# Performance work log

Measured on AMD Instinct MI355X. Metric: run time of the kernel, lower is better.

The kernel has to match this reference:

```python
import jax, jax.numpy as jnp
import numpy as np

N_HEAD = 8
D_HEAD = 32  # d_model=256 // n_head=8
SCALE = 1.0 / (D_HEAD ** 0.5)
CLIP = 10.0


def _rel_shift(x):
    # x: [qlen, klen, B, nh]; Transformer-XL relative shift along axis 1
    qlen, klen = x.shape[0], x.shape[1]
    zero_pad = jnp.zeros((qlen, 1) + x.shape[2:], dtype=x.dtype)
    x_pad = jnp.concatenate([zero_pad, x], axis=1)          # [qlen, klen+1, B, nh]
    x_pad = x_pad.reshape((klen + 1, qlen) + x.shape[2:])   # row-major reshape (torch .view)
    return x_pad[1:].reshape(x.shape)


def setup_inputs() -> dict:
    key = jax.random.key(0)
    ks = jax.random.split(key, 7)
    S, B, H = 1024, 8, 256
    return {
        "q": jax.random.normal(ks[0], (S, B, H), dtype=jnp.float32),
        "k": jax.random.normal(ks[1], (S, B, H), dtype=jnp.float32),
        "v": jax.random.normal(ks[2], (S, B, H), dtype=jnp.float32),
        "r": jax.random.normal(ks[3], (S, 1, H), dtype=jnp.float32),
        "bias_u": jax.random.normal(ks[4], (N_HEAD, D_HEAD), dtype=jnp.float32),
        "bias_v": jax.random.normal(ks[5], (N_HEAD, D_HEAD), dtype=jnp.float32),
        "mask": jax.random.randint(ks[6], (S, S, B), 0, 2).astype(jnp.bool_),
    }


def reference(q, k, v, r, bias_u, bias_v, mask):
    qlen, bsz = q.shape[0], q.shape[1]
    klen, rlen = k.shape[0], r.shape[0]
    q = q.reshape(qlen, bsz, N_HEAD, D_HEAD)
    k = k.reshape(klen, bsz, N_HEAD, D_HEAD)
    v = v.reshape(klen, bsz, N_HEAD, D_HEAD)
    r = r.reshape(rlen, N_HEAD, D_HEAD)

    AC = jnp.einsum('ibnd,jbnd->ijbn', q + bias_u, k)   # content term
    BD = jnp.einsum('ibnd,jnd->ijbn', q + bias_v, r)    # position term
    BD = _rel_shift(BD)

    score = (AC + BD) * SCALE
    score = CLIP * jnp.tanh(score)                      # clip > 0 path

    weight = jax.nn.softmax(score, axis=1)              # softmax over klen

    # mask is not None path: masked softmax of head-mean logits
    logits = score.mean(axis=-1)                        # [qlen, klen, B]
    logits = jnp.where(mask, -jnp.inf, logits)
    probs = jax.nn.softmax(logits, axis=1)

    out = jnp.einsum('ijbn,jbnd->ibnd', weight, v)
    out = out.reshape(qlen, bsz, N_HEAD * D_HEAD)
    return out, probs
```

## Files before the change

### kernel.cpp

```cpp
#include <hip/hip_runtime.h>
#include <hip/hip_fp16.h>

#define S 1024
#define B 8
#define NH 8
#define DH 32
#define HID 256
#define SCALEF 0.17677669529663687f

typedef __attribute__((ext_vector_type(8))) _Float16 f16x8;
typedef __attribute__((ext_vector_type(4))) _Float16 f16x4;
typedef __attribute__((ext_vector_type(4))) float f32x4;
#define MFMAH(a, b, c) __builtin_amdgcn_mfma_f32_16x16x32_f16(a, b, c, 0, 0, 0)

#define OFF_K_H 0
#define OFF_K_L 2560
#define OFF_VT  5120
#define OFF_RL  7680
#define OFF_RH  12800
#define OFF_P   17920
#define LDS_HF  20480

#define C_E2  0.51006978f
#define C_PWA 14.42695041f
#define C_PWB -28.85390082f

__device__ __forceinline__ void splitf16_4(const float4 x, _Float16* dh, _Float16* dl) {
  f16x4 h, l;
  h.x = (_Float16)x.x; h.y = (_Float16)x.y; h.z = (_Float16)x.z; h.w = (_Float16)x.w;
  l.x = (_Float16)(x.x - (float)h.x); l.y = (_Float16)(x.y - (float)h.y);
  l.z = (_Float16)(x.z - (float)h.z); l.w = (_Float16)(x.w - (float)h.w);
  *(f16x4*)dh = h; *(f16x4*)dl = l;
}
__device__ __forceinline__ void cvtf16_4(const float4 x, _Float16* d) {
  f16x4 h;
  h.x = (_Float16)x.x; h.y = (_Float16)x.y; h.z = (_Float16)x.z; h.w = (_Float16)x.w;
  *(f16x4*)d = h;
}

__global__ __launch_bounds__(256)
void relattn_mfma_86028194939537(const float* __restrict__ q, const float* __restrict__ k,
                                 const float* __restrict__ v, const float* __restrict__ r,
                                 const float* __restrict__ bu, const float* __restrict__ bv,
                                 float* __restrict__ out, __half* __restrict__ sws) {
  __shared__ _Float16 sm[LDS_HF];
  const int t = threadIdx.x;
  const int lane = t & 63, w = t >> 6;
  const int quad = lane >> 4, jn = lane & 15;
  const int bid = blockIdx.x;
  const int b = bid & 7, it = (bid >> 3) & 15, n = bid >> 7;
  const int i0 = it << 6, iw0 = i0 + (w << 4);
  const int colq = quad << 3;
  const int i16 = i0 >> 4;

  f16x8 qu_h, qu_l, qv_h, qv_l, qn_h, qn_l;
  {
    const float* bup = bu + n * DH + colq;
    const float* bvp = bv + n * DH + colq;
    const float* qp = q + (size_t)(iw0 + jn) * 2048 + b * HID + n * DH + colq;
    int r1 = iw0 + 1 + jn; if (r1 > S - 1) r1 = S - 1;
    const float* qp1 = q + (size_t)r1 * 2048 + b * HID + n * DH + colq;
#pragma unroll
    for (int e = 0; e < 8; ++e) {
      float xu = qp[e] + bup[e], xv = qp[e] + bvp[e], xn = qp1[e] + bvp[e];
      _Float16 h;
      h = (_Float16)xu; qu_h[e] = h; qu_l[e] = (_Float16)(xu - (float)h);
      h = (_Float16)xv; qv_h[e] = h; qv_l[e] = (_Float16)(xv - (float)h);
      h = (_Float16)xn; qn_h[e] = h; qn_l[e] = (_Float16)(xn - (float)h);
    }
  }

  const int prow = lane >> 2, pseg = lane & 3;
  __half* swsp = sws + (((size_t)(iw0 + prow) * 8 + b) * 8 + n) * 1024 + (pseg << 3);

  f32x4 out0 = {0.f, 0.f, 0.f, 0.f}, out1 = {0.f, 0.f, 0.f, 0.f};
  float ls[4] = {0.f, 0.f, 0.f, 0.f};

  {
    int j = t >> 3, d4 = (t & 7) << 2;
    const size_t g = (size_t)j * 2048 + b * HID + n * DH + d4;
    float4 kx = *(const float4*)(k + g);
    float4 vx = *(const float4*)(v + g);
    splitf16_4(kx, &sm[OFF_K_H + j * 40 + d4], &sm[OFF_K_L + j * 40 + d4]);
    sm[OFF_VT + (d4 + 0) * 40 + j] = (_Float16)vx.x;
    sm[OFF_VT + (d4 + 1) * 40 + j] = (_Float16)vx.y;
    sm[OFF_VT + (d4 + 2) * 40 + j] = (_Float16)vx.z;
    sm[OFF_VT + (d4 + 3) * 40 + j] = (_Float16)vx.w;
  }
#pragma unroll
  for (int p = 0; p < 3; ++p) {
    int ti = 2 * p + (t >> 7), row = (t >> 3) & 15, d4 = (t & 7) << 2;
    {
      int kL = 60 - i16 + ti;
      int tg = (kL << 4) + row; tg = tg < 0 ? 0 : (tg > S - 1 ? S - 1 : tg);
      float4 rv = *(const float4*)(r + (size_t)tg * HID + n * DH + d4);
      int sl = (kL + 72) & 7;
      cvtf16_4(rv, &sm[OFF_RL + (sl * 16 + row) * 40 + d4]);
    }
    {
      int kH = -i16 - 3 + ti;
      int tg = (kH << 4) - 17 + row; tg = tg < 0 ? 0 : (tg > S - 1 ? S - 1 : tg);
      float4 rv = *(const float4*)(r + (size_t)tg * HID + n * DH + d4);
      int sl = (kH + 72) & 7;
      cvtf16_4(rv, &sm[OFF_RH + (sl * 16 + row) * 40 + d4]);
    }
  }

  for (int jt = 0; jt < 32; ++jt) {
    const int j0 = jt << 5;
    __syncthreads();

    if (jt < 31) {
      int j = t >> 3, d4 = (t & 7) << 2;
      const int nbuf = ((jt + 1) & 1) * 1280;
      const size_t g = (size_t)(j0 + 32 + j) * 2048 + b * HID + n * DH + d4;
      float4 kx = *(const float4*)(k + g);
      float4 vx = *(const float4*)(v + g);
      splitf16_4(kx, &sm[OFF_K_H + nbuf + j * 40 + d4], &sm[OFF_K_L + nbuf + j * 40 + d4]);
      sm[OFF_VT + nbuf + (d4 + 0) * 40 + j] = (_Float16)vx.x;
      sm[OFF_VT + nbuf + (d4 + 1) * 40 + j] = (_Float16)vx.y;
      sm[OFF_VT + nbuf + (d4 + 2) * 40 + j] = (_Float16)vx.z;
      sm[OFF_VT + nbuf + (d4 + 3) * 40 + j] = (_Float16)vx.w;
    }
    {
      int ti = t >> 7, row = (t >> 3) & 15, d4 = (t & 7) << 2;
      {
        int kL = 66 + 2 * jt - i16 + ti;
        int tg = (kL << 4) + row; tg = tg < 0 ? 0 : (tg > S - 1 ? S - 1 : tg);
        float4 rv = *(const float4*)(r + (size_t)tg * HID + n * DH + d4);
        int sl = (kL + 72) & 7;
        cvtf16_4(rv, &sm[OFF_RL + (sl * 16 + row) * 40 + d4]);
      }
      {
        int kH = 2 * jt - i16 + 3 + ti;
        int tg = (kH << 4) - 17 + row; tg = tg < 0 ? 0 : (tg > S - 1 ? S - 1 : tg);
        float4 rv = *(const float4*)(r + (size_t)tg * HID + n * DH + d4);
        int sl = (kH + 72) & 7;
        cvtf16_4(rv, &sm[OFF_RH + (sl * 16 + row) * 40 + d4]);
      }
    }

    const int buf = (jt & 1) * 1280;
    const bool lowA = (j0 <= iw0 + 15);
    const bool highA = (j0 + 29 >= iw0);

    f32x4 ac0 = {0.f, 0.f, 0.f, 0.f}, ac1 = {0.f, 0.f, 0.f, 0.f};
    {
      f16x8 b0h = *(const f16x8*)&sm[OFF_K_H + buf + jn * 40 + colq];
      f16x8 b0l = *(const f16x8*)&sm[OFF_K_L + buf + jn * 40 + colq];
      f16x8 b1h = *(const f16x8*)&sm[OFF_K_H + buf + (16 + jn) * 40 + colq];
      f16x8 b1l = *(const f16x8*)&sm[OFF_K_L + buf + (16 + jn) * 40 + colq];
      ac0 = MFMAH(qu_h, b0h, ac0); ac0 = MFMAH(qu_h, b0l, ac0); ac0 = MFMAH(qu_l, b0h, ac0);
      ac1 = MFMAH(qu_h, b1h, ac1); ac1 = MFMAH(qu_h, b1l, ac1); ac1 = MFMAH(qu_l, b1h, ac1);
    }

    f32x4 zl0 = {0.f,0.f,0.f,0.f}, zl1 = {0.f,0.f,0.f,0.f}, zl2 = {0.f,0.f,0.f,0.f};
    f32x4 zh0 = {0.f,0.f,0.f,0.f}, zh1 = {0.f,0.f,0.f,0.f}, zh2 = {0.f,0.f,0.f,0.f};
    if (lowA) {
#pragma unroll
      for (int z = 0; z < 3; ++z) {
        int kL = 63 - i16 - w + 2 * jt + z;
        int sl = (kL + 72) & 7;
        f16x8 rr = *(const f16x8*)&sm[OFF_RL + (sl * 16 + jn) * 40 + colq];
        f32x4 acc = {0.f, 0.f, 0.f, 0.f};
        acc = MFMAH(qv_h, rr, acc); acc = MFMAH(qv_l, rr, acc);
        if (z == 0) zl0 = acc; else if (z == 1) zl1 = acc; else zl2 = acc;
      }
    }
    if (highA) {
#pragma unroll
      for (int z = 0; z < 3; ++z) {
        int kH = 2 * jt - i16 - w + z;
        int sl = (kH + 72) & 7;
        f16x8 rr = *(const f16x8*)&sm[OFF_RH + (sl * 16 + jn) * 40 + colq];
        f32x4 acc = {0.f, 0.f, 0.f, 0.f};
        acc = MFMAH(qn_h, rr, acc); acc = MFMAH(qn_l, rr, acc);
        if (z == 0) zh0 = acc; else if (z == 1) zh1 = acc; else zh2 = acc;
      }
    }

#pragma unroll
    for (int g = 0; g < 4; ++g) {
      const int qr = (quad << 2) + g;
      const int c0 = 15 - qr + jn;
      const int src = (lane & 48) | (c0 & 15);
      const bool zs = (c0 < 16);
      float lo0 = 0.f, lo1 = 0.f, hv0 = 0.f, hv1 = 0.f;
      if (lowA) {
        float a0 = __shfl(zl0[g], src, 64);
        float a1 = __shfl(zl1[g], src, 64);
        float a2 = __shfl(zl2[g], src, 64);
        lo0 = zs ? a0 : a1; lo1 = zs ? a1 : a2;
      }
      if (highA) {
        float a0 = __shfl(zh0[g], src, 64);
        float a1 = __shfl(zh1[g], src, 64);
        float a2 = __shfl(zh2[g], src, 64);
        hv0 = zs ? a0 : a1; hv1 = zs ? a1 : a2;
      }
      const int dj0 = j0 + jn - iw0 - qr;
#pragma unroll
      for (int f = 0; f < 2; ++f) {
        const int dj = dj0 + (f << 4);
        const float bd = (dj <= 0) ? (f ? lo1 : lo0) : ((dj == 1) ? 0.f : (f ? hv1 : hv0));
        const float acv = f ? ac1[g] : ac0[g];
        const float s = acv + bd;
        const float e2 = __builtin_amdgcn_exp2f(s * C_E2);
        const float tq = __builtin_amdgcn_rcpf(e2 + 1.f);
        const float pw = __builtin_amdgcn_exp2f(fmaf(tq, C_PWB, C_PWA));
        const _Float16 ph = (_Float16)pw;
        ls[g] += (float)ph;
        sm[OFF_P + w * 640 + qr * 40 + (f << 4) + jn] = ph;
      }
    }

    {
      f16x8 pa = *(const f16x8*)&sm[OFF_P + w * 640 + jn * 40 + colq];
      f16x8 v0 = *(const f16x8*)&sm[OFF_VT + buf + jn * 40 + colq];
      f16x8 v1 = *(const f16x8*)&sm[OFF_VT + buf + (16 + jn) * 40 + colq];
      out0 = MFMAH(pa, v0, out0);
      out1 = MFMAH(pa, v1, out1);
    }

    {
      f16x8 pr = *(const f16x8*)&sm[OFF_P + w * 640 + prow * 40 + (pseg << 3)];
      *(f16x8*)swsp = pr;
      swsp += 32;
    }
  }

#pragma unroll
  for (int g = 0; g < 4; ++g) {
    float s = ls[g];
    s += __shfl_xor(s, 1, 64); s += __shfl_xor(s, 2, 64);
    s += __shfl_xor(s, 4, 64); s += __shfl_xor(s, 8, 64);
    const float inv = 1.0f / s;
    const int qr = (quad << 2) + g;
    float* op = out + (size_t)(iw0 + qr) * 2048 + b * HID + n * DH;
    op[jn] = out0[g] * inv;
    op[16 + jn] = out1[g] * inv;
  }
}

__global__ __launch_bounds__(1024)
void relattn_probs_86028194939537(const __half* __restrict__ sws, const int* __restrict__ mask,
                                  float* __restrict__ probs) {
  __shared__ _Float16 ebuf[8][1032];
  __shared__ unsigned char mb[8192];
  __shared__ float psum[8][4];
  __shared__ float binv[8];
  const int t = threadIdx.x;
  const int i = blockIdx.x;
  const int tj = t & 255, bg = t >> 8;
  const int j4 = tj << 2;
  const int wl = (t >> 6) & 3;

  {
    const int4* m4 = (const int4*)(mask + (size_t)i * 8192);
#pragma unroll
    for (int u = 0; u < 2; ++u) {
      int idx = t + (u << 10);
      int4 mv = m4[idx];
      uchar4 mbv;
      mbv.x = (unsigned char)(mv.x != 0); mbv.y = (unsigned char)(mv.y != 0);
      mbv.z = (unsigned char)(mv.z != 0); mbv.w = (unsigned char)(mv.w != 0);
      *(uchar4*)&mb[idx << 2] = mbv;
    }
  }
  __syncthreads();

#pragma unroll
  for (int bb = 0; bb < 2; ++bb) {
    const int b = (bg << 1) + bb;
    float a0 = 1.f, a1 = 1.f, a2 = 1.f, a3 = 1.f;
#pragma unroll
    for (int n = 0; n < 8; ++n) {
      f16x4 pv = *(const f16x4*)(sws + (((size_t)i * 8 + b) * 8 + n) * 1024 + j4);
      a0 *= (float)pv.x; a1 *= (float)pv.y; a2 *= (float)pv.z; a3 *= (float)pv.w;
    }
    float e0 = mb[(j4 + 0) * 8 + b] ? 0.f : sqrtf(sqrtf(sqrtf(a0)));
    float e1 = mb[(j4 + 1) * 8 + b] ? 0.f : sqrtf(sqrtf(sqrtf(a1)));
    float e2 = mb[(j4 + 2) * 8 + b] ? 0.f : sqrtf(sqrtf(sqrtf(a2)));
    float e3 = mb[(j4 + 3) * 8 + b] ? 0.f : sqrtf(sqrtf(sqrtf(a3)));
    f16x4 ev;
    ev.x = (_Float16)e0; ev.y = (_Float16)e1; ev.z = (_Float16)e2; ev.w = (_Float16)e3;
    *(f16x4*)&ebuf[b][j4] = ev;
    float s = ((float)ev.x + (float)ev.y) + ((float)ev.z + (float)ev.w);
#pragma unroll
    for (int off = 32; off > 0; off >>= 1) s += __shfl_xor(s, off, 64);
    if ((t & 63) == 0) psum[b][wl] = s;
  }
  __syncthreads();
  if (t < 8) binv[t] = 1.0f / (psum[t][0] + psum[t][1] + psum[t][2] + psum[t][3]);
  __syncthreads();
#pragma unroll
  for (int u = 0; u < 2; ++u) {
    int f0 = (t << 2) + (u << 12);
    float4 o;
    o.x = (float)ebuf[(f0 + 0) & 7][(f0 + 0) >> 3] * binv[(f0 + 0) & 7];
    o.y = (float)ebuf[(f0 + 1) & 7][(f0 + 1) >> 3] * binv[(f0 + 1) & 7];
    o.z = (float)ebuf[(f0 + 2) & 7][(f0 + 2) >> 3] * binv[(f0 + 2) & 7];
    o.w = (float)ebuf[(f0 + 3) & 7][(f0 + 3) >> 3] * binv[(f0 + 3) & 7];
    *(float4*)(probs + (size_t)i * 8192 + f0) = o;
  }
}

#define TI 8
#define TJ 8
#define NTILE (S / TJ)
#define KSTR 288
#define KOFF 0
#define VOFF (TJ * KSTR)
#define BAND (2 * TJ * KSTR)
#define PROWS (TI + TJ - 1)
#define BSTR 292
#define BVR (BAND + PROWS * BSTR)
#define BUKo (BVR + PROWS * 8)
#define LDS_FL (BUKo + 64)

__global__ __launch_bounds__(256, 2)
void relattn_main_fb(const float* __restrict__ q, const float* __restrict__ k,
                     const float* __restrict__ v, const float* __restrict__ r,
                     const float* __restrict__ bias_u, const float* __restrict__ bias_v,
                     const int* __restrict__ mask, float* __restrict__ out,
                     float* __restrict__ probs_raw, float* __restrict__ ws_logits, int use_ws) {
  __shared__ float smf[LDS_FL];
  const int t = threadIdx.x;
  const int n = t & 7;
  const int il = (t >> 3) & 7;
  const int jp = t >> 6;
  const int bid = blockIdx.x;
  const int b = bid & 7;
  const int i0 = (bid >> 3) * TI;
  const int i = i0 + il;
  float qq[DH], qn[DH];
  {
    const float4* qr = (const float4*)(q + (i * B + b) * HID + n * DH);
#pragma unroll
    for (int dd = 0; dd < 8; ++dd) {
      float4 a = qr[dd];
      qq[4*dd+0] = a.x; qq[4*dd+1] = a.y; qq[4*dd+2] = a.z; qq[4*dd+3] = a.w;
    }
    if (i + 1 < S) {
      const float4* q2 = (const float4*)(q + ((i + 1) * B + b) * HID + n * DH);
#pragma unroll
      for (int dd = 0; dd < 8; ++dd) {
        float4 a = q2[dd];
        qn[4*dd+0] = a.x; qn[4*dd+1] = a.y; qn[4*dd+2] = a.z; qn[4*dd+3] = a.w;
      }
    } else {
#pragma unroll
      for (int d = 0; d < DH; ++d) qn[d] = 0.f;
    }
  }
  float oacc[DH];
#pragma unroll
  for (int d = 0; d < DH; ++d) oacc[d] = 0.f;
  float lsum = 0.f;
  for (int jt = 0; jt < NTILE; ++jt) {
    const int j0 = jt * TJ;
    const int Pstar = i0 + (TI - 1) - j0;
    const int lowBase = S - TI + j0 - i0;
    const int upBase = j0 - i0 - (TI + 1);
    __syncthreads();
    {
      int u = t;
      int row = u >> 6, c = u & 63;
      int gofs = ((j0 + row) * B + b) * HID + c * 4;
      int lofs = row * KSTR + (c >> 3) * 36 + (c & 7) * 4;
      *(float4*)(smf + KOFF + lofs) = *(const float4*)(k + gofs);
      *(float4*)(smf + VOFF + lofs) = *(const float4*)(v + gofs);
      u = t + 256; row = u >> 6; c = u & 63;
      gofs = ((j0 + row) * B + b) * HID + c * 4;
      lofs = row * KSTR + (c >> 3) * 36 + (c & 7) * 4;
      *(float4*)(smf + KOFF + lofs) = *(const float4*)(k + gofs);
      *(float4*)(smf + VOFF + lofs) = *(const float4*)(v + gofs);
    }
    for (int u = t; u < PROWS * 64; u += 256) {
      int prow = u >> 6, c = u & 63;
      int trow = (prow <= Pstar) ? (lowBase + prow) : (upBase + prow);
      float4 val = make_float4(0.f, 0.f, 0.f, 0.f);
      if ((unsigned)trow < (unsigned)S) val = *(const float4*)(r + trow * HID + c * 4);
      *(float4*)(smf + BAND + prow * BSTR + (c >> 3) * 36 + (c & 7) * 4) = val;
    }
    if (t < 64 + PROWS * 8) {
      const float4 *bb, *src;
      int slot;
      bool zero = false;
      if (t < 64) {
        int jl = t >> 3, nn = t & 7;
        bb = (const float4*)(bias_u + nn * DH);
        src = (const float4*)(k + ((j0 + jl) * B + b) * HID + nn * DH);
        slot = BUKo + jl * 8 + nn;
      } else {
        int u2 = t - 64;
        int prow = u2 >> 3, nn = u2 & 7;
        int trow = (prow <= Pstar) ? (lowBase + prow) : (upBase + prow);
        bb = (const float4*)(bias_v + nn * DH);
        if ((unsigned)trow < (unsigned)S) src = (const float4*)(r + trow * HID + nn * DH);
        else { src = bb; zero = true; }
        slot = BVR + prow * 8 + nn;
      }
      float a0 = 0.f, a1 = 0.f, a2 = 0.f, a3 = 0.f;
#pragma unroll
      for (int dd = 0; dd < 8; ++dd) {
        float4 x = bb[dd], y = src[dd];
        a0 = fmaf(x.x, y.x, a0); a1 = fmaf(x.y, y.y, a1);
        a2 = fmaf(x.z, y.z, a2); a3 = fmaf(x.w, y.w, a3);
      }
      smf[slot] = zero ? 0.f : ((a0 + a1) + (a2 + a3));
    }
    __syncthreads();
#pragma unroll
    for (int jj = 0; jj < 2; ++jj) {
      const int jl = jp * 2 + jj;
      const int jg = j0 + jl;
      const int p = jl + (TI - 1) - il;
      float a0 = 0.f, a1 = 0.f, a2 = 0.f, a3 = 0.f;
      const float4* kr = (const float4*)(smf + KOFF + jl * KSTR + n * 36);
#pragma unroll
      for (int dd = 0; dd < 8; ++dd) {
        float4 kv = kr[dd];
        a0 = fmaf(qq[4*dd+0], kv.x, a0); a1 = fmaf(qq[4*dd+1], kv.y, a1);
        a2 = fmaf(qq[4*dd+2], kv.z, a2); a3 = fmaf(qq[4*dd+3], kv.w, a3);
      }
      float ac = (a0 + a1) + (a2 + a3) + smf[BUKo + jl * 8 + n];
      float b0 = 0.f, b1 = 0.f, b2 = 0.f, b3 = 0.f;
      const float4* br = (const float4*)(smf + BAND + p * BSTR + n * 36);
      if (jg <= i) {
#pragma unroll
        for (int dd = 0; dd < 8; ++dd) {
          float4 bv4 = br[dd];
          b0 = fmaf(qq[4*dd+0], bv4.x, b0); b1 = fmaf(qq[4*dd+1], bv4.y, b1);
          b2 = fmaf(qq[4*dd+2], bv4.z, b2); b3 = fmaf(qq[4*dd+3], bv4.w, b3);
        }
      } else {
#pragma unroll
        for (int dd = 0; dd < 8; ++dd) {
          float4 bv4 = br[dd];
          b0 = fmaf(qn[4*dd+0], bv4.x, b0); b1 = fmaf(qn[4*dd+1], bv4.y, b1);
          b2 = fmaf(qn[4*dd+2], bv4.z, b2); b3 = fmaf(qn[4*dd+3], bv4.w, b3);
        }
      }
      float bd = (b0 + b1) + (b2 + b3) + smf[BVR + p * 8 + n];
      float sr = (ac + bd) * SCALEF;
      sr = fminf(fmaxf(sr, -15.f), 15.f);
      float e2 = __expf(2.f * sr);
      float scv = 10.f * (e2 - 1.f) / (e2 + 1.f);
      float ssum = scv;
      ssum += __shfl_xor(ssum, 1, 64);
      ssum += __shfl_xor(ssum, 2, 64);
      ssum += __shfl_xor(ssum, 4, 64);
      if (n == 0) {
        float logit = ssum * 0.125f;
        if (use_ws) {
          ws_logits[(i * B + b) * S + jg] = logit;
        } else {
          int gofs = (i * S + jg) * B + b;
          probs_raw[gofs] = (mask[gofs] != 0) ? -1e30f : logit;
        }
      }
      float pw = __expf(scv);
      lsum += pw;
      const float4* vr = (const float4*)(smf + VOFF + jl * KSTR + n * 36);
#pragma unroll
      for (int dd = 0; dd < 8; ++dd) {
        float4 vv = vr[dd];
        oacc[4*dd+0] = fmaf(pw, vv.x, oacc[4*dd+0]);
        oacc[4*dd+1] = fmaf(pw, vv.y, oacc[4*dd+1]);
        oacc[4*dd+2] = fmaf(pw, vv.z, oacc[4*dd+2]);
        oacc[4*dd+3] = fmaf(pw, vv.w, oacc[4*dd+3]);
      }
    }
  }
  __syncthreads();
  if (jp >= 2) {
    float* red = smf + (t - 128) * 33;
#pragma unroll
    for (int d = 0; d < DH; ++d) red[d] = oacc[d];
    red[DH] = lsum;
  }
  __syncthreads();
  if (jp < 2) {
    const float* red = smf + t * 33;
#pragma unroll
    for (int d = 0; d < DH; ++d) oacc[d] += red[d];
    lsum += red[DH];
  }
  __syncthreads();
  if (jp == 1) {
    float* red = smf + (t - 64) * 33;
#pragma unroll
    for (int d = 0; d < DH; ++d) red[d] = oacc[d];
    red[DH] = lsum;
  }
  __syncthreads();
  if (jp == 0) {
    const float* red = smf + t * 33;
#pragma unroll
    for (int d = 0; d < DH; ++d) oacc[d] += red[d];
    lsum += red[DH];
    float inv = 1.f / lsum;
    float4* orow = (float4*)(out + (i * B + b) * HID + n * DH);
#pragma unroll
    for (int dd = 0; dd < 8; ++dd) {
      float4 o4;
      o4.x = oacc[4*dd+0] * inv; o4.y = oacc[4*dd+1] * inv;
      o4.z = oacc[4*dd+2] * inv; o4.w = oacc[4*dd+3] * inv;
      orow[dd] = o4;
    }
  }
}

__global__ __launch_bounds__(256)
void relattn_norm_fb(float* __restrict__ probs, const float* __restrict__ ws_logits,
                     const int* __restrict__ mask, int use_ws) {
  const int t = threadIdx.x;
  const int bid = blockIdx.x;
  const int b = bid & 7;
  const int i = bid >> 3;
  float vals[4];
  float s = 0.f;
#pragma unroll
  for (int kk = 0; kk < 4; ++kk) {
    int j = t + 256 * kk;
    float lg;
    if (use_ws) {
      lg = ws_logits[(i * B + b) * S + j];
      if (mask[(i * S + j) * B + b] != 0) lg = -1e30f;
    } else {
      lg = probs[(i * S + j) * B + b];
    }
    vals[kk] = __expf(lg);
    s += vals[kk];
  }
#pragma unroll
  for (int off = 32; off > 0; off >>= 1) s += __shfl_down(s, off, 64);
  __shared__ float wsum[4];
  __shared__ float tot;
  if ((t & 63) == 0) wsum[t >> 6] = s;
  __syncthreads();
  if (t == 0) tot = wsum[0] + wsum[1] + wsum[2] + wsum[3];
  __syncthreads();
  float inv = 1.f / tot;
#pragma unroll
  for (int kk = 0; kk < 4; ++kk) {
    int j = t + 256 * kk;
    probs[(i * S + j) * B + b] = vals[kk] * inv;
  }
}

extern "C" void kernel_launch(void* const* d_in, const int* in_sizes, int n_in,
                              void* d_out, int out_size, void* d_ws, size_t ws_size,
                              hipStream_t stream) {
  const float* q  = (const float*)d_in[0];
  const float* k  = (const float*)d_in[1];
  const float* v  = (const float*)d_in[2];
  const float* r  = (const float*)d_in[3];
  const float* bu = (const float*)d_in[4];
  const float* bv = (const float*)d_in[5];
  const int* mask = (const int*)d_in[6];
  float* out = (float*)d_out;
  float* probs = out + S * B * HID;

  const size_t WS_NEED = (size_t)S * S * B * NH * sizeof(__half);
  if (ws_size >= WS_NEED) {
    __half* sws = (__half*)d_ws;
    relattn_mfma_86028194939537<<<dim3(1024), dim3(256), 0, stream>>>(
        q, k, v, r, bu, bv, out, sws);
    relattn_probs_86028194939537<<<dim3(1024), dim3(1024), 0, stream>>>(sws, mask, probs);
  } else {
    float* wsl = (float*)d_ws;
    const int use_ws = (ws_size >= (size_t)S * S * B * sizeof(float)) ? 1 : 0;
    relattn_main_fb<<<dim3((S / TI) * B), dim3(256), 0, stream>>>(
        q, k, v, r, bu, bv, mask, out, probs, wsl, use_ws);
    relattn_norm_fb<<<dim3(S * B), dim3(256), 0, stream>>>(probs, wsl, mask, use_ws);
  }
}
```

Measured before the change: 286.0 us.

## Swizzle V transpose in LDS, skip unused R tiles, reduce shuffles, add priorities

Applies an XOR swizzle to the transposed V tile in LDS, on both the write and the read side, to reduce bank conflicts on the scattered per-element stores. It also skips loading R tiles for the low and high diagonals when later iterations will not use them. Before each cross-lane shuffle it selects between neighbouring accumulators, so each shuffle step does two shuffles instead of three. It wraps the MFMA sections in s_setprio hints. The risks are that the swizzle mapping must match exactly between writer and reader, and that the new skip conditions must cover every tile the compute loop reads.

```diff
diff --git a/kernel.cpp b/kernel.cpp
--- a/kernel.cpp
+++ b/kernel.cpp
@@ -53,6 +53,13 @@
   const int colq = quad << 3;
   const int i16 = i0 >> 4;
 
+  const int jstage = t >> 3, dstage = (t & 7) << 2;
+  const int jsw = jstage ^ ((t & 3) << 3);
+  const int vcolsw = colq ^ (((jn >> 2) & 3) << 3);
+
+  const int jtL_last = (i0 + 63) >> 5;
+  const bool proH = (i0 <= 125);
+
   f16x8 qu_h, qu_l, qv_h, qv_l, qn_h, qn_l;
   {
     const float* bup = bu + n * DH + colq;
@@ -77,15 +84,14 @@
   float ls[4] = {0.f, 0.f, 0.f, 0.f};
 
   {
-    int j = t >> 3, d4 = (t & 7) << 2;
-    const size_t g = (size_t)j * 2048 + b * HID + n * DH + d4;
+    const size_t g = (size_t)jstage * 2048 + b * HID + n * DH + dstage;
     float4 kx = *(const float4*)(k + g);
     float4 vx = *(const float4*)(v + g);
-    splitf16_4(kx, &sm[OFF_K_H + j * 40 + d4], &sm[OFF_K_L + j * 40 + d4]);
-    sm[OFF_VT + (d4 + 0) * 40 + j] = (_Float16)vx.x;
-    sm[OFF_VT + (d4 + 1) * 40 + j] = (_Float16)vx.y;
-    sm[OFF_VT + (d4 + 2) * 40 + j] = (_Float16)vx.z;
-    sm[OFF_VT + (d4 + 3) * 40 + j] = (_Float16)vx.w;
+    splitf16_4(kx, &sm[OFF_K_H + jstage * 40 + dstage], &sm[OFF_K_L + jstage * 40 + dstage]);
+    sm[OFF_VT + (dstage + 0) * 40 + jsw] = (_Float16)vx.x;
+    sm[OFF_VT + (dstage + 1) * 40 + jsw] = (_Float16)vx.y;
+    sm[OFF_VT + (dstage + 2) * 40 + jsw] = (_Float16)vx.z;
+    sm[OFF_VT + (dstage + 3) * 40 + jsw] = (_Float16)vx.w;
   }
 #pragma unroll
   for (int p = 0; p < 3; ++p) {
@@ -97,7 +103,7 @@
       int sl = (kL + 72) & 7;
       cvtf16_4(rv, &sm[OFF_RL + (sl * 16 + row) * 40 + d4]);
     }
-    {
+    if (proH) {
       int kH = -i16 - 3 + ti;
       int tg = (kH << 4) - 17 + row; tg = tg < 0 ? 0 : (tg > S - 1 ? S - 1 : tg);
       float4 rv = *(const float4*)(r + (size_t)tg * HID + n * DH + d4);
@@ -111,27 +117,27 @@
     __syncthreads();
 
     if (jt < 31) {
-      int j = t >> 3, d4 = (t & 7) << 2;
       const int nbuf = ((jt + 1) & 1) * 1280;
-      const size_t g = (size_t)(j0 + 32 + j) * 2048 + b * HID + n * DH + d4;
+      const size_t g = (size_t)(j0 + 32 + jstage) * 2048 + b * HID + n * DH + dstage;
       float4 kx = *(const float4*)(k + g);
       float4 vx = *(const float4*)(v + g);
-      splitf16_4(kx, &sm[OFF_K_H + nbuf + j * 40 + d4], &sm[OFF_K_L + nbuf + j * 40 + d4]);
-      sm[OFF_VT + nbuf + (d4 + 0) * 40 + j] = (_Float16)vx.x;
-      sm[OFF_VT + nbuf + (d4 + 1) * 40 + j] = (_Float16)vx.y;
-      sm[OFF_VT + nbuf + (d4 + 2) * 40 + j] = (_Float16)vx.z;
-      sm[OFF_VT + nbuf + (d4 + 3) * 40 + j] = (_Float16)vx.w;
+      splitf16_4(kx, &sm[OFF_K_H + nbuf + jstage * 40 + dstage],
+                 &sm[OFF_K_L + nbuf + jstage * 40 + dstage]);
+      sm[OFF_VT + nbuf + (dstage + 0) * 40 + jsw] = (_Float16)vx.x;
+      sm[OFF_VT + nbuf + (dstage + 1) * 40 + jsw] = (_Float16)vx.y;
+      sm[OFF_VT + nbuf + (dstage + 2) * 40 + jsw] = (_Float16)vx.z;
+      sm[OFF_VT + nbuf + (dstage + 3) * 40 + jsw] = (_Float16)vx.w;
     }
     {
       int ti = t >> 7, row = (t >> 3) & 15, d4 = (t & 7) << 2;
-      {
+      if (jt <= jtL_last) {
         int kL = 66 + 2 * jt - i16 + ti;
         int tg = (kL << 4) + row; tg = tg < 0 ? 0 : (tg > S - 1 ? S - 1 : tg);
         float4 rv = *(const float4*)(r + (size_t)tg * HID + n * DH + d4);
         int sl = (kL + 72) & 7;
         cvtf16_4(rv, &sm[OFF_RL + (sl * 16 + row) * 40 + d4]);
       }
-      {
+      if (32 * jt >= i0 - 125) {
         int kH = 2 * jt - i16 + 3 + ti;
         int tg = (kH << 4) - 17 + row; tg = tg < 0 ? 0 : (tg > S - 1 ? S - 1 : tg);
         float4 rv = *(const float4*)(r + (size_t)tg * HID + n * DH + d4);
@@ -144,6 +150,7 @@
     const bool lowA = (j0 <= iw0 + 15);
     const bool highA = (j0 + 29 >= iw0);
 
+    __builtin_amdgcn_s_setprio(1);
     f32x4 ac0 = {0.f, 0.f, 0.f, 0.f}, ac1 = {0.f, 0.f, 0.f, 0.f};
     {
       f16x8 b0h = *(const f16x8*)&sm[OFF_K_H + buf + jn * 40 + colq];
@@ -178,25 +185,26 @@
         if (z == 0) zh0 = acc; else if (z == 1) zh1 = acc; else zh2 = acc;
       }
     }
+    __builtin_amdgcn_s_setprio(0);
 
 #pragma unroll
     for (int g = 0; g < 4; ++g) {
       const int qr = (quad << 2) + g;
       const int c0 = 15 - qr + jn;
       const int src = (lane & 48) | (c0 & 15);
-      const bool zs = (c0 < 16);
+      const bool pred = (jn >= 15 - qr);
       float lo0 = 0.f, lo1 = 0.f, hv0 = 0.f, hv1 = 0.f;
       if (lowA) {
-        float a0 = __shfl(zl0[g], src, 64);
-        float a1 = __shfl(zl1[g], src, 64);
-        float a2 = __shfl(zl2[g], src, 64);
-        lo0 = zs ? a0 : a1; lo1 = zs ? a1 : a2;
+        float vA = pred ? zl0[g] : zl1[g];
+        float vB = pred ? zl1[g] : zl2[g];
+        lo0 = __shfl(vA, src, 64);
+        lo1 = __shfl(vB, src, 64);
       }
       if (highA) {
-        float a0 = __shfl(zh0[g], src, 64);
-        float a1 = __shfl(zh1[g], src, 64);
-        float a2 = __shfl(zh2[g], src, 64);
-        hv0 = zs ? a0 : a1; hv1 = zs ? a1 : a2;
+        float vA = pred ? zh0[g] : zh1[g];
+        float vB = pred ? zh1[g] : zh2[g];
+        hv0 = __shfl(vA, src, 64);
+        hv1 = __shfl(vB, src, 64);
       }
       const int dj0 = j0 + jn - iw0 - qr;
 #pragma unroll
@@ -214,13 +222,15 @@
       }
     }
 
+    __builtin_amdgcn_s_setprio(1);
     {
       f16x8 pa = *(const f16x8*)&sm[OFF_P + w * 640 + jn * 40 + colq];
-      f16x8 v0 = *(const f16x8*)&sm[OFF_VT + buf + jn * 40 + colq];
-      f16x8 v1 = *(const f16x8*)&sm[OFF_VT + buf + (16 + jn) * 40 + colq];
+      f16x8 v0 = *(const f16x8*)&sm[OFF_VT + buf + jn * 40 + vcolsw];
+      f16x8 v1 = *(const f16x8*)&sm[OFF_VT + buf + (16 + jn) * 40 + vcolsw];
       out0 = MFMAH(pa, v0, out0);
       out1 = MFMAH(pa, v1, out1);
     }
+    __builtin_amdgcn_s_setprio(0);
 
     {
       f16x8 pr = *(const f16x8*)&sm[OFF_P + w * 640 + prow * 40 + (pseg << 3)];
```

Result: slower. 305.9 us (+7.0%).
